# Optimization experiments

Measured on AMD Instinct MI355X. Metric: run time of the kernel, lower is better.

Reference implementation:

```python
import jax, jax.numpy as jnp
import numpy as np

B, S, D_MODEL = 2, 2048, 1024
HEADS = 16
DK = D_MODEL // HEADS  # 64
Q_RANK, RANK = 6, 2
ROPE_BASE = 10000.0


def _xavier(key, shape):
    # torch nn.init.xavier_uniform_ on weight (out,in); stored here as (in,out)
    fan_in, fan_out = shape
    a = (6.0 / (fan_in + fan_out)) ** 0.5
    return jax.random.uniform(key, shape, jnp.float32, -a, a)


def setup_inputs() -> dict:
    key = jax.random.key(0)
    ks = jax.random.split(key, 10)
    inp = {
        "q": jax.random.normal(ks[0], (B, S, D_MODEL), jnp.float32),
        "k": jax.random.normal(ks[1], (B, S, D_MODEL), jnp.float32),
        "v": jax.random.normal(ks[2], (B, S, D_MODEL), jnp.float32),
        # causal mask; mask==0 -> -inf in scores
        "mask": jnp.tril(jnp.ones((S, S), dtype=bool))[None, None],
        "W_Aq": _xavier(ks[3], (D_MODEL, Q_RANK * HEADS)),
        "W_Ak": _xavier(ks[4], (D_MODEL, RANK * HEADS)),
        "W_Av": _xavier(ks[5], (D_MODEL, RANK * HEADS)),
        "W_Bq": _xavier(ks[6], (D_MODEL, Q_RANK * DK)),
        "W_Bk": _xavier(ks[7], (D_MODEL, RANK * DK)),
        "W_Bv": _xavier(ks[8], (D_MODEL, RANK * DK)),
        "Wo": _xavier(ks[9], (D_MODEL, D_MODEL)),
    }
    return inp


def _rotary_cos_sin(seq_len, dim):
    inv_freq = 1.0 / (ROPE_BASE ** (jnp.arange(0, dim, 2, dtype=jnp.float32) / dim))
    freqs = jnp.outer(jnp.arange(seq_len, dtype=jnp.float32), inv_freq)  # [S, dim/2]
    return jnp.cos(freqs)[None, :, None, :], jnp.sin(freqs)[None, :, None, :]


def _apply_rotary(x, cos, sin):
    # x: [B, S, R, dk]; rotate-half style RoPE
    d = x.shape[-1] // 2
    x1, x2 = x[..., :d], x[..., d:]
    return jnp.concatenate([x1 * cos + x2 * sin, -x1 * sin + x2 * cos], axis=-1)


def reference(q, k, v, mask, W_Aq, W_Ak, W_Av, W_Bq, W_Bk, W_Bv, Wo):
    Bn, Sn, D = q.shape
    # low-rank factor projections
    A_q = (q @ W_Aq).reshape(Bn, Sn, HEADS, Q_RANK)
    A_k = (k @ W_Ak).reshape(Bn, Sn, HEADS, RANK)
    A_v = (v @ W_Av).reshape(Bn, Sn, HEADS, RANK)
    B_q = (q @ W_Bq).reshape(Bn, Sn, Q_RANK, DK)
    B_k = (k @ W_Bk).reshape(Bn, Sn, RANK, DK)
    B_v = (v @ W_Bv).reshape(Bn, Sn, RANK, DK)
    cos, sin = _rotary_cos_sin(Sn, DK)
    B_q = _apply_rotary(B_q, cos, sin)
    B_k = _apply_rotary(B_k, cos, sin)
    # reconstruct per-head q/k/v: [B,H,S,dk]
    qh = jnp.einsum("bshr,bsrd->bhsd", A_q, B_q) / Q_RANK
    kh = jnp.einsum("bshr,bsrd->bhsd", A_k, B_k) / RANK
    vh = jnp.einsum("bshr,bsrd->bhsd", A_v, B_v) / RANK
    # NOTE: original divides by d_k (not sqrt(d_k)) -- faithful to source
    score = jnp.einsum("bhqd,bhkd->bhqk", qh, kh) / DK
    score = jnp.where(mask, score, -jnp.inf)
    # dropout is identity (eval / dropout=0.0)
    att = jax.nn.softmax(score, axis=-1)
    out = jnp.einsum("bhqk,bhkd->bqhd", att, vh).reshape(Bn, Sn, D)
    return out @ Wo
```

## Files before the change

### kernel.cpp

```cpp
#include <hip/hip_runtime.h>
#include <hip/hip_bf16.h>


typedef __attribute__((ext_vector_type(8))) short short8;
typedef __attribute__((ext_vector_type(4))) float floatx4;

#define MFMA16(a, b, c) __builtin_amdgcn_mfma_f32_16x16x32_bf16(a, b, c, 0, 0, 0)

__device__ __forceinline__ float b2f(short s) {
    unsigned int u = ((unsigned int)(unsigned short)s) << 16;
    float f; __builtin_memcpy(&f, &u, 4); return f;
}
__device__ __forceinline__ unsigned short bfbits(float x) {
    __hip_bfloat16 h = __float2bfloat16(x);
    unsigned short u; __builtin_memcpy(&u, &h, 2); return u;
}

__device__ __forceinline__ float wsrc(int n, int k,
                                      const float* __restrict__ Aq, const float* __restrict__ Bq,
                                      const float* __restrict__ Ak, const float* __restrict__ Bk,
                                      const float* __restrict__ Av, const float* __restrict__ Bv,
                                      const float* __restrict__ Wo) {
    if (n < 96) return Aq[(size_t)k * 96 + n];
    if (n < 480) return Bq[(size_t)k * 384 + (n - 96)];
    if (n < 512) return 0.f;
    if (n < 544) return Ak[(size_t)k * 32 + (n - 512)];
    if (n < 672) return Bk[(size_t)k * 128 + (n - 544)];
    if (n < 768) return 0.f;
    if (n < 800) return Av[(size_t)k * 32 + (n - 768)];
    if (n < 928) return Bv[(size_t)k * 128 + (n - 800)];
    if (n < 1024) return 0.f;
    return Wo[(size_t)k * 1024 + (n - 1024)];
}

__global__ __launch_bounds__(256) void pack_wT_kernel(const float* __restrict__ Aq,
                                                      const float* __restrict__ Bq,
                                                      const float* __restrict__ Ak,
                                                      const float* __restrict__ Bk,
                                                      const float* __restrict__ Av,
                                                      const float* __restrict__ Bv,
                                                      const float* __restrict__ Wo,
                                                      __hip_bfloat16* __restrict__ outBase) {
    __shared__ float tile[64][65];
    int k0 = blockIdx.x * 64, n0 = blockIdx.y * 64;
    int tid = threadIdx.x;
#pragma unroll
    for (int p = 0; p < 16; ++p) {
        int idx = p * 256 + tid;
        int kl = idx >> 6, nl = idx & 63;
        tile[kl][nl] = wsrc(n0 + nl, k0 + kl, Aq, Bq, Ak, Bk, Av, Bv, Wo);
    }
    __syncthreads();
#pragma unroll
    for (int p = 0; p < 16; ++p) {
        int idx = p * 256 + tid;
        int nl = idx >> 6, kl = idx & 63;
        outBase[(size_t)(n0 + nl) * 1024 + k0 + kl] = __float2bfloat16(tile[kl][nl]);
    }
}

__global__ __launch_bounds__(256) void gemm3_kernel(const float* __restrict__ q,
                                                    const float* __restrict__ k,
                                                    const float* __restrict__ v,
                                                    const __hip_bfloat16* __restrict__ WT,
                                                    __hip_bfloat16* __restrict__ Pq,
                                                    __hip_bfloat16* __restrict__ Pk,
                                                    __hip_bfloat16* __restrict__ Pv) {
    __shared__ __align__(16) __hip_bfloat16 As[128][72];
    __shared__ __align__(16) __hip_bfloat16 Bs[128][72];
    int lin = blockIdx.x;
    int t = (lin >> 3) & 7;
    int m0 = ((lin & 7) + ((lin >> 6) << 3)) * 128;
    const float* A; __hip_bfloat16* C; int N, n0, wrow;
    if (t < 4)      { A = q; C = Pq; N = 512; n0 = t * 128;        wrow = t * 128; }
    else if (t < 6) { A = k; C = Pk; N = 256; n0 = (t - 4) * 128;  wrow = 512 + (t - 4) * 128; }
    else            { A = v; C = Pv; N = 256; n0 = (t - 6) * 128;  wrow = 768 + (t - 6) * 128; }
    int tid = threadIdx.x;
    int wave = tid >> 6, lane = tid & 63, quad = lane >> 4, l15 = lane & 15;
    int wm = wave >> 1, wn = wave & 1;
    floatx4 acc[4][4];
#pragma unroll
    for (int mt = 0; mt < 4; ++mt)
#pragma unroll
        for (int nt = 0; nt < 4; ++nt) acc[mt][nt] = (floatx4){0.f, 0.f, 0.f, 0.f};

    for (int k0 = 0; k0 < 1024; k0 += 64) {
#pragma unroll
        for (int pp = 0; pp < 8; ++pp) {
            int idx = pp * 256 + tid;
            int row = idx >> 4, c4 = (idx & 15) * 4;
            float4 av = *(const float4*)(A + (size_t)(m0 + row) * 1024 + k0 + c4);
            ushort4 bv;
            bv.x = bfbits(av.x); bv.y = bfbits(av.y); bv.z = bfbits(av.z); bv.w = bfbits(av.w);
            *(ushort4*)&As[row][c4] = bv;
        }
#pragma unroll
        for (int pp = 0; pp < 4; ++pp) {
            int idx = pp * 256 + tid;
            int row = idx >> 3, c8 = (idx & 7) * 8;
            *(uint4*)&Bs[row][c8] = *(const uint4*)(WT + (size_t)(wrow + row) * 1024 + k0 + c8);
        }
        __syncthreads();
#pragma unroll
        for (int ks = 0; ks < 64; ks += 32) {
            short8 af[4], bf[4];
#pragma unroll
            for (int t2 = 0; t2 < 4; ++t2) {
                af[t2] = *(const short8*)&As[wm * 64 + t2 * 16 + l15][ks + quad * 8];
                bf[t2] = *(const short8*)&Bs[wn * 64 + t2 * 16 + l15][ks + quad * 8];
            }
#pragma unroll
            for (int mt = 0; mt < 4; ++mt)
#pragma unroll
                for (int nt = 0; nt < 4; ++nt)
                    acc[mt][nt] = MFMA16(af[mt], bf[nt], acc[mt][nt]);
        }
        __syncthreads();
    }
#pragma unroll
    for (int mt = 0; mt < 4; ++mt)
#pragma unroll
        for (int nt = 0; nt < 4; ++nt)
#pragma unroll
            for (int r = 0; r < 4; ++r) {
                int row = m0 + wm * 64 + mt * 16 + quad * 4 + r;
                int col = n0 + wn * 64 + nt * 16 + l15;
                C[(size_t)row * N + col] = __float2bfloat16(acc[mt][nt][r]);
            }
}

__global__ __launch_bounds__(256) void gemm_out_kernel(const __hip_bfloat16* __restrict__ A,
                                                       const __hip_bfloat16* __restrict__ BT,
                                                       float* __restrict__ C) {
    __shared__ __align__(16) __hip_bfloat16 As[128][72];
    __shared__ __align__(16) __hip_bfloat16 Bs[128][72];
    int lin = blockIdx.x;
    int n0 = ((lin >> 3) & 7) * 128;
    int m0 = ((lin & 7) + ((lin >> 6) << 3)) * 128;
    int tid = threadIdx.x;
    int wave = tid >> 6, lane = tid & 63, quad = lane >> 4, l15 = lane & 15;
    int wm = wave >> 1, wn = wave & 1;
    floatx4 acc[4][4];
#pragma unroll
    for (int mt = 0; mt < 4; ++mt)
#pragma unroll
        for (int nt = 0; nt < 4; ++nt) acc[mt][nt] = (floatx4){0.f, 0.f, 0.f, 0.f};

    for (int k0 = 0; k0 < 1024; k0 += 64) {
#pragma unroll
        for (int pp = 0; pp < 4; ++pp) {
            int idx = pp * 256 + tid;
            int row = idx >> 3, c8 = (idx & 7) * 8;
            *(uint4*)&As[row][c8] = *(const uint4*)(A + (size_t)(m0 + row) * 1024 + k0 + c8);
            *(uint4*)&Bs[row][c8] = *(const uint4*)(BT + (size_t)(n0 + row) * 1024 + k0 + c8);
        }
        __syncthreads();
#pragma unroll
        for (int ks = 0; ks < 64; ks += 32) {
            short8 af[4], bf[4];
#pragma unroll
            for (int t2 = 0; t2 < 4; ++t2) {
                af[t2] = *(const short8*)&As[wm * 64 + t2 * 16 + l15][ks + quad * 8];
                bf[t2] = *(const short8*)&Bs[wn * 64 + t2 * 16 + l15][ks + quad * 8];
            }
#pragma unroll
            for (int mt = 0; mt < 4; ++mt)
#pragma unroll
                for (int nt = 0; nt < 4; ++nt)
                    acc[mt][nt] = MFMA16(af[mt], bf[nt], acc[mt][nt]);
        }
        __syncthreads();
    }
#pragma unroll
    for (int mt = 0; mt < 4; ++mt)
#pragma unroll
        for (int nt = 0; nt < 4; ++nt)
#pragma unroll
            for (int r = 0; r < 4; ++r) {
                int row = m0 + wm * 64 + mt * 16 + quad * 4 + r;
                int col = n0 + wn * 64 + nt * 16 + l15;
                C[(size_t)row * 1024 + col] = acc[mt][nt][r];
            }
}

__global__ __launch_bounds__(256) void combine_vt_kernel(const __hip_bfloat16* __restrict__ Pq,
                                                         const __hip_bfloat16* __restrict__ Pk,
                                                         const __hip_bfloat16* __restrict__ Pv,
                                                         __hip_bfloat16* __restrict__ qh,
                                                         __hip_bfloat16* __restrict__ kh,
                                                         __hip_bfloat16* __restrict__ vT) {
    __shared__ __align__(16) __hip_bfloat16 LAq[16][96];
    __shared__ __align__(16) __hip_bfloat16 LAk[16][32];
    __shared__ __align__(16) __hip_bfloat16 LAv[16][32];
    __shared__ __align__(16) __hip_bfloat16 LBq[16][6][72];
    __shared__ __align__(16) __hip_bfloat16 LBk[16][2][72];
    __shared__ __align__(16) __hip_bfloat16 LBv[16][2][72];
    int tid = threadIdx.x;
    int token0 = blockIdx.x * 16;
    int b = token0 >> 11, s0 = token0 & 2047, bh0 = b * 16;

    for (int i = tid; i < 16 * 512; i += 256) {
        int s = i >> 9, c = i & 511;
        __hip_bfloat16 val = Pq[(size_t)(token0 + s) * 512 + c];
        if (c < 96) LAq[s][c] = val;
        else if (c < 480) LBq[s][(c - 96) >> 6][(c - 96) & 63] = val;
    }
    for (int i = tid; i < 16 * 256; i += 256) {
        int s = i >> 8, c = i & 255;
        __hip_bfloat16 vk = Pk[(size_t)(token0 + s) * 256 + c];
        __hip_bfloat16 vv = Pv[(size_t)(token0 + s) * 256 + c];
        if (c < 32) { LAk[s][c] = vk; LAv[s][c] = vv; }
        else if (c < 160) {
            LBk[s][(c - 32) >> 6][(c - 32) & 63] = vk;
            LBv[s][(c - 32) >> 6][(c - 32) & 63] = vv;
        }
    }
    __syncthreads();
    for (int i = tid; i < 4096; i += 256) {
        int s = i >> 8, rr = (i >> 5) & 7, d = i & 31;
        float inv = __expf(-(float)d * 0.28782313662425576f);
        float rev = (float)(s0 + s) * inv * 0.15915494309189535f;
        rev -= floorf(rev);
        float sn = __builtin_amdgcn_sinf(rev);
        float cs = __builtin_amdgcn_cosf(rev);
        if (rr < 6) {
            float x1 = b2f(*(short*)&LBq[s][rr][d]), x2 = b2f(*(short*)&LBq[s][rr][d + 32]);
            LBq[s][rr][d] = __float2bfloat16(x1 * cs + x2 * sn);
            LBq[s][rr][d + 32] = __float2bfloat16(-x1 * sn + x2 * cs);
        } else {
            int r2 = rr - 6;
            float x1 = b2f(*(short*)&LBk[s][r2][d]), x2 = b2f(*(short*)&LBk[s][r2][d + 32]);
            LBk[s][r2][d] = __float2bfloat16(x1 * cs + x2 * sn);
            LBk[s][r2][d + 32] = __float2bfloat16(-x1 * sn + x2 * cs);
        }
    }
    __syncthreads();
    const float QSCALE = 1.4426950408889634f / 768.0f;
    {
        int s = tid >> 4, h = tid & 15;
        float aq[6], ak0, ak1;
#pragma unroll
        for (int r = 0; r < 6; ++r) aq[r] = b2f(*(short*)&LAq[s][h * 6 + r]);
        ak0 = b2f(*(short*)&LAk[s][h * 2]);
        ak1 = b2f(*(short*)&LAk[s][h * 2 + 1]);
        size_t obase = ((size_t)(bh0 + h) * 2048 + s0 + s) * 64;
#pragma unroll
        for (int dc = 0; dc < 64; dc += 8) {
            float accq[8] = {0, 0, 0, 0, 0, 0, 0, 0};
#pragma unroll
            for (int r = 0; r < 6; ++r) {
                short8 bq = *(const short8*)&LBq[s][r][dc];
#pragma unroll
                for (int e = 0; e < 8; ++e) accq[e] += aq[r] * b2f(bq[e]);
            }
            short8 bk0 = *(const short8*)&LBk[s][0][dc];
            short8 bk1 = *(const short8*)&LBk[s][1][dc];
            ushort outq[8], outk[8];
#pragma unroll
            for (int e = 0; e < 8; ++e) {
                outq[e] = bfbits(accq[e] * QSCALE);
                outk[e] = bfbits(ak0 * b2f(bk0[e]) + ak1 * b2f(bk1[e]));
            }
            *(uint4*)((__hip_bfloat16*)qh + obase + dc) = *(uint4*)outq;
            *(uint4*)((__hip_bfloat16*)kh + obase + dc) = *(uint4*)outk;
        }
    }
    {
        int s = tid & 15, dg = tid >> 4;
#pragma unroll
        for (int h = 0; h < 16; ++h) {
            float a0 = b2f(*(short*)&LAv[s][h * 2]) * 0.5f;
            float a1 = b2f(*(short*)&LAv[s][h * 2 + 1]) * 0.5f;
#pragma unroll
            for (int dd = 0; dd < 4; ++dd) {
                int d = dg * 4 + dd;
                float val = a0 * b2f(*(short*)&LBv[s][0][d]) + a1 * b2f(*(short*)&LBv[s][1][d]);
                vT[((size_t)(bh0 + h) * 64 + d) * 2048 + s0 + s] = __float2bfloat16(val);
            }
        }
    }
}

__global__ __launch_bounds__(256) void flash_kernel(const __hip_bfloat16* __restrict__ qh,
                                                    const __hip_bfloat16* __restrict__ kh,
                                                    const __hip_bfloat16* __restrict__ vT,
                                                    __hip_bfloat16* __restrict__ att) {
    int lin = blockIdx.x + (blockIdx.y << 5);
    int bh = ((lin & 7) << 2) | ((lin >> 3) & 3);
    int qi = 31 - (lin >> 5);
    int tid = threadIdx.x;
    int wave = tid >> 6, lane = tid & 63, quad = lane >> 4, l15 = lane & 15;
    int q0 = qi * 64;
    __shared__ __align__(16) __hip_bfloat16 Ks[64][72];
    __shared__ __align__(16) __hip_bfloat16 Vts[64][72];
    __shared__ __align__(16) __hip_bfloat16 Ps[4][16][72];

    const __hip_bfloat16* qrow = qh + ((size_t)bh * 2048 + q0 + wave * 16 + l15) * 64 + quad * 8;
    short8 aq0 = *(const short8*)(qrow);
    short8 aq1 = *(const short8*)(qrow + 32);

    floatx4 o[4];
#pragma unroll
    for (int nt = 0; nt < 4; ++nt) o[nt] = (floatx4){0.f, 0.f, 0.f, 0.f};
    float rs[4] = {0.f, 0.f, 0.f, 0.f};

    for (int j = 0; j <= qi; ++j) {
        int k0 = j * 64;
#pragma unroll
        for (int pp = 0; pp < 2; ++pp) {
            int idx = pp * 256 + tid;
            int row = idx >> 3, c8 = (idx & 7) * 8;
            *(uint4*)&Ks[row][c8] = *(const uint4*)(kh + ((size_t)bh * 2048 + k0 + row) * 64 + c8);
            *(uint4*)&Vts[row][c8] = *(const uint4*)(vT + ((size_t)bh * 64 + row) * 2048 + k0 + c8);
        }
        __syncthreads();

        floatx4 s[4];
#pragma unroll
        for (int nt = 0; nt < 4; ++nt) s[nt] = (floatx4){0.f, 0.f, 0.f, 0.f};
#pragma unroll
        for (int nt = 0; nt < 4; ++nt) {
            short8 bk0 = *(const short8*)&Ks[nt * 16 + l15][quad * 8];
            short8 bk1 = *(const short8*)&Ks[nt * 16 + l15][32 + quad * 8];
            s[nt] = MFMA16(aq0, bk0, s[nt]);
            s[nt] = MFMA16(aq1, bk1, s[nt]);
        }
        if (j == qi) {
            int rbase = wave * 16 + quad * 4;
#pragma unroll
            for (int nt = 0; nt < 4; ++nt) {
                int cl = nt * 16 + l15;
#pragma unroll
                for (int r = 0; r < 4; ++r)
                    if (cl > rbase + r) s[nt][r] = -__builtin_inff();
            }
        }
        float pv[4][4];
#pragma unroll
        for (int nt = 0; nt < 4; ++nt)
#pragma unroll
            for (int r = 0; r < 4; ++r) {
                pv[nt][r] = exp2f(s[nt][r]);
                rs[r] += pv[nt][r];
            }
#pragma unroll
        for (int nt = 0; nt < 4; ++nt)
#pragma unroll
            for (int r = 0; r < 4; ++r)
                Ps[wave][quad * 4 + r][nt * 16 + l15] = __float2bfloat16(pv[nt][r]);
        __builtin_amdgcn_s_waitcnt(0xC07F);
        short8 pa0 = *(const short8*)&Ps[wave][l15][quad * 8];
        short8 pa1 = *(const short8*)&Ps[wave][l15][32 + quad * 8];
#pragma unroll
        for (int nt = 0; nt < 4; ++nt) {
            short8 bv0 = *(const short8*)&Vts[nt * 16 + l15][quad * 8];
            short8 bv1 = *(const short8*)&Vts[nt * 16 + l15][32 + quad * 8];
            o[nt] = MFMA16(pa0, bv0, o[nt]);
            o[nt] = MFMA16(pa1, bv1, o[nt]);
        }
        __syncthreads();
    }
    float l_i[4];
#pragma unroll
    for (int r = 0; r < 4; ++r) {
        float x = rs[r];
        x += __shfl_xor(x, 1, 64);
        x += __shfl_xor(x, 2, 64);
        x += __shfl_xor(x, 4, 64);
        x += __shfl_xor(x, 8, 64);
        l_i[r] = x;
    }
    int b = bh >> 4, h = bh & 15;
    size_t obase = ((size_t)b * 2048 + q0 + wave * 16 + quad * 4) * 1024 + h * 64;
#pragma unroll
    for (int nt = 0; nt < 4; ++nt)
#pragma unroll
        for (int r = 0; r < 4; ++r)
            att[obase + (size_t)r * 1024 + nt * 16 + l15] = __float2bfloat16(o[nt][r] / l_i[r]);
}

extern "C" void kernel_launch(void* const* d_in, const int* in_sizes, int n_in,
                              void* d_out, int out_size, void* d_ws, size_t ws_size,
                              hipStream_t stream) {
    const float* q = (const float*)d_in[0];
    const float* k = (const float*)d_in[1];
    const float* v = (const float*)d_in[2];
    const float* W_Aq = (const float*)d_in[4];
    const float* W_Ak = (const float*)d_in[5];
    const float* W_Av = (const float*)d_in[6];
    const float* W_Bq = (const float*)d_in[7];
    const float* W_Bk = (const float*)d_in[8];
    const float* W_Bv = (const float*)d_in[9];
    const float* Wo = (const float*)d_in[10];
    float* out = (float*)d_out;

    char* w = (char*)d_ws;
    __hip_bfloat16* qh  = (__hip_bfloat16*)(w + 0);
    __hip_bfloat16* kh  = (__hip_bfloat16*)(w + 8388608);
    __hip_bfloat16* vT  = (__hip_bfloat16*)(w + 16777216);
    __hip_bfloat16* WT  = (__hip_bfloat16*)(w + 25165824);
    __hip_bfloat16* WoT = WT + (size_t)1024 * 1024;
    __hip_bfloat16* Pq  = (__hip_bfloat16*)(w + 29360128);
    __hip_bfloat16* Pk  = (__hip_bfloat16*)(w + 33554432);
    __hip_bfloat16* Pv  = (__hip_bfloat16*)(w + 35651584);
    __hip_bfloat16* att = (__hip_bfloat16*)(w + 37748736);

    pack_wT_kernel<<<dim3(16, 32), 256, 0, stream>>>(W_Aq, W_Bq, W_Ak, W_Bk, W_Av, W_Bv, Wo, WT);
    gemm3_kernel<<<256, 256, 0, stream>>>(q, k, v, WT, Pq, Pk, Pv);
    combine_vt_kernel<<<256, 256, 0, stream>>>(Pq, Pk, Pv, qh, kh, vT);
    flash_kernel<<<dim3(32, 32), 256, 0, stream>>>(qh, kh, vT, att);
    gemm_out_kernel<<<256, 256, 0, stream>>>(att, WoT, out);
}
```

Baseline: 255.7 us.

## Double-buffer GEMM shared tiles and split flash attention into 32-row blocks

Both projection GEMMs now prefetch the next K-tile into registers while computing on the current shared-memory buffer, alternating between two LDS buffers with one barrier per iteration. This is meant to hide global load latency behind the MFMA work. The flash attention kernel moves from 64-query-row blocks of 4 waves to 32-row blocks of 2 waves, with twice as many blocks, to improve load balance across the causal triangle and raise occupancy. The cost is more LDS per GEMM block, since launch_bounds is set to (256,1). Smaller attention blocks also reload each K/V tile for half as many query rows.

```diff
diff --git a/kernel.cpp b/kernel.cpp
--- a/kernel.cpp
+++ b/kernel.cpp
@@ -59,15 +59,15 @@
     }
 }
 
-__global__ __launch_bounds__(256) void gemm3_kernel(const float* __restrict__ q,
-                                                    const float* __restrict__ k,
-                                                    const float* __restrict__ v,
-                                                    const __hip_bfloat16* __restrict__ WT,
-                                                    __hip_bfloat16* __restrict__ Pq,
-                                                    __hip_bfloat16* __restrict__ Pk,
-                                                    __hip_bfloat16* __restrict__ Pv) {
-    __shared__ __align__(16) __hip_bfloat16 As[128][72];
-    __shared__ __align__(16) __hip_bfloat16 Bs[128][72];
+__global__ __launch_bounds__(256, 1) void gemm3_kernel(const float* __restrict__ q,
+                                                       const float* __restrict__ k,
+                                                       const float* __restrict__ v,
+                                                       const __hip_bfloat16* __restrict__ WT,
+                                                       __hip_bfloat16* __restrict__ Pq,
+                                                       __hip_bfloat16* __restrict__ Pk,
+                                                       __hip_bfloat16* __restrict__ Pv) {
+    __shared__ __align__(16) __hip_bfloat16 As[2][128][72];
+    __shared__ __align__(16) __hip_bfloat16 Bs[2][128][72];
     int lin = blockIdx.x;
     int t = (lin >> 3) & 7;
     int m0 = ((lin & 7) + ((lin >> 6) << 3)) * 128;
@@ -84,30 +84,61 @@
 #pragma unroll
         for (int nt = 0; nt < 4; ++nt) acc[mt][nt] = (floatx4){0.f, 0.f, 0.f, 0.f};
 
-    for (int k0 = 0; k0 < 1024; k0 += 64) {
-#pragma unroll
-        for (int pp = 0; pp < 8; ++pp) {
-            int idx = pp * 256 + tid;
-            int row = idx >> 4, c4 = (idx & 15) * 4;
-            float4 av = *(const float4*)(A + (size_t)(m0 + row) * 1024 + k0 + c4);
-            ushort4 bv;
-            bv.x = bfbits(av.x); bv.y = bfbits(av.y); bv.z = bfbits(av.z); bv.w = bfbits(av.w);
-            *(ushort4*)&As[row][c4] = bv;
-        }
-#pragma unroll
-        for (int pp = 0; pp < 4; ++pp) {
-            int idx = pp * 256 + tid;
-            int row = idx >> 3, c8 = (idx & 7) * 8;
-            *(uint4*)&Bs[row][c8] = *(const uint4*)(WT + (size_t)(wrow + row) * 1024 + k0 + c8);
-        }
+    float4 avr[8];
+    uint4 bvr[4];
+#pragma unroll
+    for (int pp = 0; pp < 8; ++pp) {
+        int idx = pp * 256 + tid;
+        int row = idx >> 4, c4 = (idx & 15) * 4;
+        avr[pp] = *(const float4*)(A + (size_t)(m0 + row) * 1024 + c4);
+    }
+#pragma unroll
+    for (int pp = 0; pp < 4; ++pp) {
+        int idx = pp * 256 + tid;
+        int row = idx >> 3, c8 = (idx & 7) * 8;
+        bvr[pp] = *(const uint4*)(WT + (size_t)(wrow + row) * 1024 + c8);
+    }
+#pragma unroll
+    for (int pp = 0; pp < 8; ++pp) {
+        int idx = pp * 256 + tid;
+        int row = idx >> 4, c4 = (idx & 15) * 4;
+        ushort4 bv;
+        bv.x = bfbits(avr[pp].x); bv.y = bfbits(avr[pp].y);
+        bv.z = bfbits(avr[pp].z); bv.w = bfbits(avr[pp].w);
+        *(ushort4*)&As[0][row][c4] = bv;
+    }
+#pragma unroll
+    for (int pp = 0; pp < 4; ++pp) {
+        int idx = pp * 256 + tid;
+        int row = idx >> 3, c8 = (idx & 7) * 8;
+        *(uint4*)&Bs[0][row][c8] = bvr[pp];
+    }
+
+    for (int i = 0; i < 16; ++i) {
+        int buf = i & 1;
         __syncthreads();
+        if (i < 15) {
+            int k0n = (i + 1) * 64;
+#pragma unroll
+            for (int pp = 0; pp < 8; ++pp) {
+                int idx = pp * 256 + tid;
+                int row = idx >> 4, c4 = (idx & 15) * 4;
+                avr[pp] = *(const float4*)(A + (size_t)(m0 + row) * 1024 + k0n + c4);
+            }
+#pragma unroll
+            for (int pp = 0; pp < 4; ++pp) {
+                int idx = pp * 256 + tid;
+                int row = idx >> 3, c8 = (idx & 7) * 8;
+                bvr[pp] = *(const uint4*)(WT + (size_t)(wrow + row) * 1024 + k0n + c8);
+            }
+        }
 #pragma unroll
         for (int ks = 0; ks < 64; ks += 32) {
             short8 af[4], bf[4];
 #pragma unroll
             for (int t2 = 0; t2 < 4; ++t2) {
-                af[t2] = *(const short8*)&As[wm * 64 + t2 * 16 + l15][ks + quad * 8];
-                bf[t2] = *(const short8*)&Bs[wn * 64 + t2 * 16 + l15][ks + quad * 8];
+                af[t2] = *(const short8*)&As[buf][wm * 64 + t2 * 16 + l15][ks + quad * 8];
+                bf[t2] = *(const short8*)&Bs[buf][wn * 64 + t2 * 16 + l15][ks + quad * 8];
             }
 #pragma unroll
             for (int mt = 0; mt < 4; ++mt)
@@ -115,7 +146,23 @@
                 for (int nt = 0; nt < 4; ++nt)
                     acc[mt][nt] = MFMA16(af[mt], bf[nt], acc[mt][nt]);
         }
-        __syncthreads();
+        if (i < 15) {
+#pragma unroll
+            for (int pp = 0; pp < 8; ++pp) {
+                int idx = pp * 256 + tid;
+                int row = idx >> 4, c4 = (idx & 15) * 4;
+                ushort4 bv;
+                bv.x = bfbits(avr[pp].x); bv.y = bfbits(avr[pp].y);
+                bv.z = bfbits(avr[pp].z); bv.w = bfbits(avr[pp].w);
+                *(ushort4*)&As[buf ^ 1][row][c4] = bv;
+            }
+#pragma unroll
+            for (int pp = 0; pp < 4; ++pp) {
+                int idx = pp * 256 + tid;
+                int row = idx >> 3, c8 = (idx & 7) * 8;
+                *(uint4*)&Bs[buf ^ 1][row][c8] = bvr[pp];
+            }
+        }
     }
 #pragma unroll
     for (int mt = 0; mt < 4; ++mt)
@@ -129,11 +176,11 @@
             }
 }
 
-__global__ __launch_bounds__(256) void gemm_out_kernel(const __hip_bfloat16* __restrict__ A,
-                                                       const __hip_bfloat16* __restrict__ BT,
-                                                       float* __restrict__ C) {
-    __shared__ __align__(16) __hip_bfloat16 As[128][72];
-    __shared__ __align__(16) __hip_bfloat16 Bs[128][72];
+__global__ __launch_bounds__(256, 1) void gemm_out_kernel(const __hip_bfloat16* __restrict__ A,
+                                                          const __hip_bfloat16* __restrict__ BT,
+                                                          float* __restrict__ C) {
+    __shared__ __align__(16) __hip_bfloat16 As[2][128][72];
+    __shared__ __align__(16) __hip_bfloat16 Bs[2][128][72];
     int lin = blockIdx.x;
     int n0 = ((lin >> 3) & 7) * 128;
     int m0 = ((lin & 7) + ((lin >> 6) << 3)) * 128;
@@ -146,22 +193,42 @@
 #pragma unroll
         for (int nt = 0; nt < 4; ++nt) acc[mt][nt] = (floatx4){0.f, 0.f, 0.f, 0.f};
 
-    for (int k0 = 0; k0 < 1024; k0 += 64) {
-#pragma unroll
-        for (int pp = 0; pp < 4; ++pp) {
-            int idx = pp * 256 + tid;
-            int row = idx >> 3, c8 = (idx & 7) * 8;
-            *(uint4*)&As[row][c8] = *(const uint4*)(A + (size_t)(m0 + row) * 1024 + k0 + c8);
-            *(uint4*)&Bs[row][c8] = *(const uint4*)(BT + (size_t)(n0 + row) * 1024 + k0 + c8);
-        }
+    uint4 avr[4], bvr[4];
+#pragma unroll
+    for (int pp = 0; pp < 4; ++pp) {
+        int idx = pp * 256 + tid;
+        int row = idx >> 3, c8 = (idx & 7) * 8;
+        avr[pp] = *(const uint4*)(A + (size_t)(m0 + row) * 1024 + c8);
+        bvr[pp] = *(const uint4*)(BT + (size_t)(n0 + row) * 1024 + c8);
+    }
+#pragma unroll
+    for (int pp = 0; pp < 4; ++pp) {
+        int idx = pp * 256 + tid;
+        int row = idx >> 3, c8 = (idx & 7) * 8;
+        *(uint4*)&As[0][row][c8] = avr[pp];
+        *(uint4*)&Bs[0][row][c8] = bvr[pp];
+    }
+
+    for (int i = 0; i < 16; ++i) {
+        int buf = i & 1;
         __syncthreads();
+        if (i < 15) {
+            int k0n = (i + 1) * 64;
+#pragma unroll
+            for (int pp = 0; pp < 4; ++pp) {
+                int idx = pp * 256 + tid;
+                int row = idx >> 3, c8 = (idx & 7) * 8;
+                avr[pp] = *(const uint4*)(A + (size_t)(m0 + row) * 1024 + k0n + c8);
+                bvr[pp] = *(const uint4*)(BT + (size_t)(n0 + row) * 1024 + k0n + c8);
+            }
+        }
 #pragma unroll
         for (int ks = 0; ks < 64; ks += 32) {
             short8 af[4], bf[4];
 #pragma unroll
             for (int t2 = 0; t2 < 4; ++t2) {
-                af[t2] = *(const short8*)&As[wm * 64 + t2 * 16 + l15][ks + quad * 8];
-                bf[t2] = *(const short8*)&Bs[wn * 64 + t2 * 16 + l15][ks + quad * 8];
+                af[t2] = *(const short8*)&As[buf][wm * 64 + t2 * 16 + l15][ks + quad * 8];
+                bf[t2] = *(const short8*)&Bs[buf][wn * 64 + t2 * 16 + l15][ks + quad * 8];
             }
 #pragma unroll
             for (int mt = 0; mt < 4; ++mt)
@@ -169,7 +236,15 @@
                 for (int nt = 0; nt < 4; ++nt)
                     acc[mt][nt] = MFMA16(af[mt], bf[nt], acc[mt][nt]);
         }
-        __syncthreads();
+        if (i < 15) {
+#pragma unroll
+            for (int pp = 0; pp < 4; ++pp) {
+                int idx = pp * 256 + tid;
+                int row = idx >> 3, c8 = (idx & 7) * 8;
+                *(uint4*)&As[buf ^ 1][row][c8] = avr[pp];
+                *(uint4*)&Bs[buf ^ 1][row][c8] = bvr[pp];
+            }
+        }
     }
 #pragma unroll
     for (int mt = 0; mt < 4; ++mt)
@@ -281,19 +356,20 @@
     }
 }
 
-__global__ __launch_bounds__(256) void flash_kernel(const __hip_bfloat16* __restrict__ qh,
+__global__ __launch_bounds__(128) void flash_kernel(const __hip_bfloat16* __restrict__ qh,
                                                     const __hip_bfloat16* __restrict__ kh,
                                                     const __hip_bfloat16* __restrict__ vT,
                                                     __hip_bfloat16* __restrict__ att) {
-    int lin = blockIdx.x + (blockIdx.y << 5);
+    int lin = blockIdx.x;
     int bh = ((lin & 7) << 2) | ((lin >> 3) & 3);
-    int qi = 31 - (lin >> 5);
+    int qt = 63 - (lin >> 5);
+    int q0 = qt * 32;
     int tid = threadIdx.x;
     int wave = tid >> 6, lane = tid & 63, quad = lane >> 4, l15 = lane & 15;
-    int q0 = qi * 64;
+    int jmax = (q0 + 31) >> 6;
     __shared__ __align__(16) __hip_bfloat16 Ks[64][72];
     __shared__ __align__(16) __hip_bfloat16 Vts[64][72];
-    __shared__ __align__(16) __hip_bfloat16 Ps[4][16][72];
+    __shared__ __align__(16) __hip_bfloat16 Ps[2][16][72];
 
     const __hip_bfloat16* qrow = qh + ((size_t)bh * 2048 + q0 + wave * 16 + l15) * 64 + quad * 8;
     short8 aq0 = *(const short8*)(qrow);
@@ -304,11 +380,11 @@
     for (int nt = 0; nt < 4; ++nt) o[nt] = (floatx4){0.f, 0.f, 0.f, 0.f};
     float rs[4] = {0.f, 0.f, 0.f, 0.f};
 
-    for (int j = 0; j <= qi; ++j) {
+    for (int j = 0; j <= jmax; ++j) {
         int k0 = j * 64;
 #pragma unroll
-        for (int pp = 0; pp < 2; ++pp) {
-            int idx = pp * 256 + tid;
+        for (int pp = 0; pp < 4; ++pp) {
+            int idx = pp * 128 + tid;
             int row = idx >> 3, c8 = (idx & 7) * 8;
             *(uint4*)&Ks[row][c8] = *(const uint4*)(kh + ((size_t)bh * 2048 + k0 + row) * 64 + c8);
             *(uint4*)&Vts[row][c8] = *(const uint4*)(vT + ((size_t)bh * 64 + row) * 2048 + k0 + c8);
@@ -325,14 +401,14 @@
             s[nt] = MFMA16(aq0, bk0, s[nt]);
             s[nt] = MFMA16(aq1, bk1, s[nt]);
         }
-        if (j == qi) {
-            int rbase = wave * 16 + quad * 4;
+        if (j == jmax) {
+            int row_abs = q0 + wave * 16 + quad * 4;
 #pragma unroll
             for (int nt = 0; nt < 4; ++nt) {
-                int cl = nt * 16 + l15;
+                int kcol = k0 + nt * 16 + l15;
 #pragma unroll
                 for (int r = 0; r < 4; ++r)
-                    if (cl > rbase + r) s[nt][r] = -__builtin_inff();
+                    if (kcol > row_abs + r) s[nt][r] = -__builtin_inff();
             }
         }
         float pv[4][4];
@@ -408,6 +484,6 @@
     pack_wT_kernel<<<dim3(16, 32), 256, 0, stream>>>(W_Aq, W_Bq, W_Ak, W_Bk, W_Av, W_Bv, Wo, WT);
     gemm3_kernel<<<256, 256, 0, stream>>>(q, k, v, WT, Pq, Pk, Pv);
     combine_vt_kernel<<<256, 256, 0, stream>>>(Pq, Pk, Pv, qh, kh, vT);
-    flash_kernel<<<dim3(32, 32), 256, 0, stream>>>(qh, kh, vT, att);
+    flash_kernel<<<2048, 128, 0, stream>>>(qh, kh, vT, att);
     gemm_out_kernel<<<256, 256, 0, stream>>>(att, WoT, out);
 }
```

New measurement: 270.7 us. 1.06x slower.
